# Kernel tuning notes

Hardware: AMD Instinct MI355X
Metric: run time of the kernel (lower is better)

## Reference

```python
import jax, jax.numpy as jnp
import numpy as np

# 18000 genes, 50 SNPs per gene (900k SNPs total), each gene block has layersize 16
B, G, K, L = 32, 18000, 50, 16
N_SNPS = G * K


def setup_inputs() -> dict:
    key = jax.random.key(0)
    k1, k2, k3, k4, k5 = jax.random.split(key, 5)
    x = jax.random.normal(k1, (B, N_SNPS), dtype=jnp.float32)
    # gene_scaling_layer: diagonal 1x1 blocks -> per-SNP scale + bias, Identity activation
    scale_w = jax.random.normal(k2, (N_SNPS,), dtype=jnp.float32)
    scale_b = jax.random.normal(k3, (N_SNPS,), dtype=jnp.float32) * 0.01
    # block-sparse weights: one [1, L] weight per (snp, gene) edge, grouped per gene -> [G, K, L]
    W = jax.random.normal(k4, (G, K, L), dtype=jnp.float32) * (1.0 / np.sqrt(K))
    b = jax.random.normal(k5, (G, L), dtype=jnp.float32) * 0.01
    # SNP indices feeding each gene (consecutive assignment, as in the torch construction loop)
    snp_index = jnp.arange(N_SNPS, dtype=jnp.int32).reshape(G, K)
    return {"x": x, "scale_w": scale_w, "scale_b": scale_b, "W": W, "b": b, "snp_index": snp_index}


def reference(x, scale_w, scale_b, W, b, snp_index):
    # scaling layer (diagonal block-sparse linear, identity activation, no dropout at eval)
    xs = x * scale_w + scale_b                      # [B, N_SNPS]
    # gather SNP features per gene block (irregular access pattern)
    xg = xs[:, snp_index]                           # [B, G, K]
    # block-sparse GEMM: each gene sums its incident SNP edge weights
    out = jnp.einsum("bgk,gkl->bgl", xg, W) + b     # [B, G, L]
    out = jax.nn.relu(out)
    return out.reshape(out.shape[0], -1)            # [B, G*L]
```

## Files before the change

kernel.cpp:

```cpp
#include <hip/hip_runtime.h>


#define B_ 32
#define G_ 18000
#define K_ 50
#define L_ 16
#define NS_ (G_ * K_)
#define GT 4
#define COLS (GT * K_)
#define Q_ (COLS / 4)
#define XS_STRIDE 204
#define THREADS_ 256

__global__ __launch_bounds__(THREADS_, 4)
void gene_model_kernel(const float* __restrict__ x,
                       const float* __restrict__ sw,
                       const float* __restrict__ sb,
                       const float* __restrict__ W,
                       const float* __restrict__ bias,
                       const int*   __restrict__ sidx,
                       float*       __restrict__ out) {
  __shared__ float xs_lds[B_ * XS_STRIDE];
  __shared__ float swc[COLS];
  __shared__ float sbc[COLS];
  __shared__ int   idxc[COLS];

  const int tid = (int)threadIdx.x;
  const int g0  = (int)blockIdx.x * GT;

  if (tid < COLS) {
    const int idx = sidx[g0 * K_ + tid];
    idxc[tid] = idx;
    swc[tid]  = sw[idx];
    sbc[tid]  = sb[idx];
  }
  __syncthreads();

  for (int i = tid; i < B_ * Q_; i += THREADS_) {
    const int r  = i / Q_;
    const int c4 = (i - r * Q_) * 4;
    const float* __restrict__ xr = x + (size_t)r * NS_;
    const int4   iv = *reinterpret_cast<const int4*>(&idxc[c4]);
    const float4 sv = *reinterpret_cast<const float4*>(&swc[c4]);
    const float4 bv = *reinterpret_cast<const float4*>(&sbc[c4]);
    float4 v;
    v.x = fmaf(xr[iv.x], sv.x, bv.x);
    v.y = fmaf(xr[iv.y], sv.y, bv.y);
    v.z = fmaf(xr[iv.z], sv.z, bv.z);
    v.w = fmaf(xr[iv.w], sv.w, bv.w);
    *reinterpret_cast<float4*>(&xs_lds[r * XS_STRIDE + c4]) = v;
  }
  __syncthreads();

  const int wave = __builtin_amdgcn_readfirstlane(tid >> 6);
  const int lane = tid & 63;
  const int g    = g0 + wave;
  const int b    = lane & 31;
  const int l0   = (lane >> 5) * 8;

  const float* __restrict__ Wg  = W + (size_t)g * (K_ * L_) + l0;
  const float* __restrict__ xsp = &xs_lds[b * XS_STRIDE + wave * K_];

  float acc[8];
  {
    const float4 bv0 = *reinterpret_cast<const float4*>(bias + (size_t)g * L_ + l0);
    const float4 bv1 = *reinterpret_cast<const float4*>(bias + (size_t)g * L_ + l0 + 4);
    acc[0] = bv0.x; acc[1] = bv0.y; acc[2] = bv0.z; acc[3] = bv0.w;
    acc[4] = bv1.x; acc[5] = bv1.y; acc[6] = bv1.z; acc[7] = bv1.w;
  }

#pragma unroll 5
  for (int k = 0; k < K_; ++k) {
    const float  xv = xsp[k];
    const float4 w0 = *reinterpret_cast<const float4*>(Wg + k * L_);
    const float4 w1 = *reinterpret_cast<const float4*>(Wg + k * L_ + 4);
    acc[0] = fmaf(xv, w0.x, acc[0]);
    acc[1] = fmaf(xv, w0.y, acc[1]);
    acc[2] = fmaf(xv, w0.z, acc[2]);
    acc[3] = fmaf(xv, w0.w, acc[3]);
    acc[4] = fmaf(xv, w1.x, acc[4]);
    acc[5] = fmaf(xv, w1.y, acc[5]);
    acc[6] = fmaf(xv, w1.z, acc[6]);
    acc[7] = fmaf(xv, w1.w, acc[7]);
  }

  float4 o0, o1;
  o0.x = fmaxf(acc[0], 0.f); o0.y = fmaxf(acc[1], 0.f);
  o0.z = fmaxf(acc[2], 0.f); o0.w = fmaxf(acc[3], 0.f);
  o1.x = fmaxf(acc[4], 0.f); o1.y = fmaxf(acc[5], 0.f);
  o1.z = fmaxf(acc[6], 0.f); o1.w = fmaxf(acc[7], 0.f);

  float* op = out + (size_t)b * (G_ * L_) + (size_t)g * L_ + l0;
  *reinterpret_cast<float4*>(op)     = o0;
  *reinterpret_cast<float4*>(op + 4) = o1;
}

extern "C" void kernel_launch(void* const* d_in, const int* in_sizes, int n_in,
                              void* d_out, int out_size, void* d_ws, size_t ws_size,
                              hipStream_t stream) {
  const float* x    = (const float*)d_in[0];
  const float* sw   = (const float*)d_in[1];
  const float* sb   = (const float*)d_in[2];
  const float* W    = (const float*)d_in[3];
  const float* bias = (const float*)d_in[4];
  const int*   sidx = (const int*)d_in[5];
  float*       out  = (float*)d_out;

  dim3 grid(G_ / GT);
  dim3 block(THREADS_);
  gene_model_kernel<<<grid, block, 0, stream>>>(x, sw, sb, W, bias, sidx, out);
}
```

Baseline: 291.7 us.

## Halve genes per block, split L across waves, drop LDS staging, nontemporal stores

Each block now handles two genes instead of four. Each gene's 16 outputs are split across two waves of four columns each, so every thread keeps four accumulators instead of eight. The scale/bias/index staging in LDS and its barrier are removed: each thread loads indices and gathers sw/sb directly, and the gather loop is fully unrolled. Output uses nontemporal stores, and launch bounds ask for higher occupancy. The trade-off is redundant sw/sb global loads across the 32 batch rows and twice as many blocks.

```diff
diff --git a/kernel.cpp b/kernel.cpp
--- a/kernel.cpp
+++ b/kernel.cpp
@@ -6,13 +6,16 @@
 #define K_ 50
 #define L_ 16
 #define NS_ (G_ * K_)
-#define GT 4
+#define GT 2
 #define COLS (GT * K_)
-#define Q_ (COLS / 4)
-#define XS_STRIDE 204
+#define QPR (COLS / 4)
+#define SLOTS (B_ * QPR)
+#define XS_STRIDE 108
 #define THREADS_ 256
 
-__global__ __launch_bounds__(THREADS_, 4)
+typedef float f32x4_ __attribute__((ext_vector_type(4)));
+
+__global__ __launch_bounds__(THREADS_, 6)
 void gene_model_kernel(const float* __restrict__ x,
                        const float* __restrict__ sw,
                        const float* __restrict__ sb,
@@ -21,78 +24,57 @@
                        const int*   __restrict__ sidx,
                        float*       __restrict__ out) {
   __shared__ float xs_lds[B_ * XS_STRIDE];
-  __shared__ float swc[COLS];
-  __shared__ float sbc[COLS];
-  __shared__ int   idxc[COLS];
 
   const int tid = (int)threadIdx.x;
   const int g0  = (int)blockIdx.x * GT;
+  const int* __restrict__ idxbase = sidx + g0 * K_;
 
-  if (tid < COLS) {
-    const int idx = sidx[g0 * K_ + tid];
-    idxc[tid] = idx;
-    swc[tid]  = sw[idx];
-    sbc[tid]  = sb[idx];
-  }
-  __syncthreads();
-
-  for (int i = tid; i < B_ * Q_; i += THREADS_) {
-    const int r  = i / Q_;
-    const int c4 = (i - r * Q_) * 4;
-    const float* __restrict__ xr = x + (size_t)r * NS_;
-    const int4   iv = *reinterpret_cast<const int4*>(&idxc[c4]);
-    const float4 sv = *reinterpret_cast<const float4*>(&swc[c4]);
-    const float4 bv = *reinterpret_cast<const float4*>(&sbc[c4]);
-    float4 v;
-    v.x = fmaf(xr[iv.x], sv.x, bv.x);
-    v.y = fmaf(xr[iv.y], sv.y, bv.y);
-    v.z = fmaf(xr[iv.z], sv.z, bv.z);
-    v.w = fmaf(xr[iv.w], sv.w, bv.w);
-    *reinterpret_cast<float4*>(&xs_lds[r * XS_STRIDE + c4]) = v;
+#pragma unroll 4
+  for (int j = 0; j < 4; ++j) {
+    const int i = tid + j * THREADS_;
+    if (i < SLOTS) {
+      const int r  = i / QPR;
+      const int c4 = (i - r * QPR) * 4;
+      const int4 iv = *reinterpret_cast<const int4*>(idxbase + c4);
+      const float* __restrict__ xr = x + (size_t)r * NS_;
+      float4 v;
+      v.x = fmaf(xr[iv.x], sw[iv.x], sb[iv.x]);
+      v.y = fmaf(xr[iv.y], sw[iv.y], sb[iv.y]);
+      v.z = fmaf(xr[iv.z], sw[iv.z], sb[iv.z]);
+      v.w = fmaf(xr[iv.w], sw[iv.w], sb[iv.w]);
+      *reinterpret_cast<float4*>(&xs_lds[r * XS_STRIDE + c4]) = v;
+    }
   }
   __syncthreads();
 
   const int wave = __builtin_amdgcn_readfirstlane(tid >> 6);
   const int lane = tid & 63;
-  const int g    = g0 + wave;
+  const int gl   = wave >> 1;
+  const int g    = g0 + gl;
   const int b    = lane & 31;
-  const int l0   = (lane >> 5) * 8;
+  const int l0   = (wave & 1) * 8 + (lane >> 5) * 4;
 
   const float* __restrict__ Wg  = W + (size_t)g * (K_ * L_) + l0;
-  const float* __restrict__ xsp = &xs_lds[b * XS_STRIDE + wave * K_];
+  const float* __restrict__ xsp = &xs_lds[b * XS_STRIDE + gl * K_];
 
-  float acc[8];
-  {
-    const float4 bv0 = *reinterpret_cast<const float4*>(bias + (size_t)g * L_ + l0);
-    const float4 bv1 = *reinterpret_cast<const float4*>(bias + (size_t)g * L_ + l0 + 4);
-    acc[0] = bv0.x; acc[1] = bv0.y; acc[2] = bv0.z; acc[3] = bv0.w;
-    acc[4] = bv1.x; acc[5] = bv1.y; acc[6] = bv1.z; acc[7] = bv1.w;
+  float4 acc = *reinterpret_cast<const float4*>(bias + (size_t)g * L_ + l0);
+
+#pragma unroll 10
+  for (int k = 0; k < K_; ++k) {
+    const float  xv = xsp[k];
+    const float4 w4 = *reinterpret_cast<const float4*>(Wg + k * L_);
+    acc.x = fmaf(xv, w4.x, acc.x);
+    acc.y = fmaf(xv, w4.y, acc.y);
+    acc.z = fmaf(xv, w4.z, acc.z);
+    acc.w = fmaf(xv, w4.w, acc.w);
   }
 
-#pragma unroll 5
-  for (int k = 0; k < K_; ++k) {
-    const float  xv = xsp[k];
-    const float4 w0 = *reinterpret_cast<const float4*>(Wg + k * L_);
-    const float4 w1 = *reinterpret_cast<const float4*>(Wg + k * L_ + 4);
-    acc[0] = fmaf(xv, w0.x, acc[0]);
-    acc[1] = fmaf(xv, w0.y, acc[1]);
-    acc[2] = fmaf(xv, w0.z, acc[2]);
-    acc[3] = fmaf(xv, w0.w, acc[3]);
-    acc[4] = fmaf(xv, w1.x, acc[4]);
-    acc[5] = fmaf(xv, w1.y, acc[5]);
-    acc[6] = fmaf(xv, w1.z, acc[6]);
-    acc[7] = fmaf(xv, w1.w, acc[7]);
-  }
-
-  float4 o0, o1;
-  o0.x = fmaxf(acc[0], 0.f); o0.y = fmaxf(acc[1], 0.f);
-  o0.z = fmaxf(acc[2], 0.f); o0.w = fmaxf(acc[3], 0.f);
-  o1.x = fmaxf(acc[4], 0.f); o1.y = fmaxf(acc[5], 0.f);
-  o1.z = fmaxf(acc[6], 0.f); o1.w = fmaxf(acc[7], 0.f);
+  f32x4_ o;
+  o.x = fmaxf(acc.x, 0.f); o.y = fmaxf(acc.y, 0.f);
+  o.z = fmaxf(acc.z, 0.f); o.w = fmaxf(acc.w, 0.f);
 
   float* op = out + (size_t)b * (G_ * L_) + (size_t)g * L_ + l0;
-  *reinterpret_cast<float4*>(op)     = o0;
-  *reinterpret_cast<float4*>(op + 4) = o1;
+  __builtin_nontemporal_store(o, reinterpret_cast<f32x4_*>(op));
 }
 
 extern "C" void kernel_launch(void* const* d_in, const int* in_sizes, int n_in,
```

New measurement: 340.2 us. +16.6%, slower.
